# Kernel optimization log

Measured on AMD Instinct MI355X. Metric: run time of the kernel, lower is better.

Reference implementation:

```python
import jax, jax.numpy as jnp
import numpy as np
from jax import lax

K = 3
PAD = 1

def setup_inputs() -> dict:
    key = jax.random.key(0)
    ks = jax.random.split(key, 5)
    B, C, H, W, O = 4, 128, 128, 128, 256
    x = jax.random.normal(ks[0], (B, C, H, W), dtype=jnp.float32)
    w_off = jax.random.normal(ks[1], (3 * K * K, C, K, K), dtype=jnp.float32) * 0.05
    b_off = jnp.zeros((3 * K * K,), dtype=jnp.float32)
    w_dw = jax.random.normal(ks[2], (C, 1, K, K), dtype=jnp.float32) * 0.2
    b_dw = jnp.zeros((C,), dtype=jnp.float32)
    w_pw = jax.random.normal(ks[3], (O, C), dtype=jnp.float32) * (1.0 / np.sqrt(C))
    b_pw = jnp.zeros((O,), dtype=jnp.float32)
    return {"x": x, "w_off": w_off, "b_off": b_off, "w_dw": w_dw,
            "b_dw": b_dw, "w_pw": w_pw, "b_pw": b_pw}

def _dcn_forward(x, w_off, b_off, w_dw, b_dw, w_pw, b_pw):
    B, C, H, W = x.shape
    K2 = K * K
    # offset/mask conv (stride 1, pad 1) -> [B, 3*K*K, H, W]
    om = lax.conv_general_dilated(
        x, w_off, window_strides=(1, 1), padding=[(PAD, PAD), (PAD, PAD)],
        dimension_numbers=("NCHW", "OIHW", "NCHW")) + b_off[None, :, None, None]
    off = om[:, : 2 * K2]                      # [B, 2*K2, H, W]
    mask = jax.nn.sigmoid(om[:, 2 * K2:])      # [B, K2, H, W]
    dy = off[:, 0::2]                          # [B, K2, H, W] (y offsets)
    dx = off[:, 1::2]                          # [B, K2, H, W] (x offsets)
    # base sampling grid per kernel tap
    ky, kx = jnp.meshgrid(jnp.arange(K), jnp.arange(K), indexing="ij")
    ky = (ky.reshape(-1) - PAD).astype(x.dtype)   # [K2]
    kx = (kx.reshape(-1) - PAD).astype(x.dtype)
    py = jnp.arange(H, dtype=x.dtype)[None, None, :, None] + ky[None, :, None, None] + dy
    px = jnp.arange(W, dtype=x.dtype)[None, None, None, :] + kx[None, :, None, None] + dx
    y0 = jnp.floor(py); x0 = jnp.floor(px)
    wy = py - y0;       wx = px - x0

    def gather(yc, xc):
        # yc, xc: [B, K2, H, W] float corner coords; zero outside bounds
        valid = ((yc >= 0) & (yc < H) & (xc >= 0) & (xc < W)).astype(x.dtype)
        yi = jnp.clip(yc, 0, H - 1).astype(jnp.int32)
        xi = jnp.clip(xc, 0, W - 1).astype(jnp.int32)
        idx = yi * W + xi                       # [B, K2, H, W]
        def per_b(xb, ib):
            # xb: [C, H, W]; ib: [K2, H, W] -> [C, K2, H, W]
            return jnp.take(xb.reshape(C, -1), ib.reshape(-1), axis=1).reshape(C, K2, H, W)
        v = jax.vmap(per_b)(x, idx)             # [B, C, K2, H, W]
        return v * valid[:, None]

    val = (gather(y0, x0) * ((1 - wy) * (1 - wx))[:, None]
           + gather(y0, x0 + 1) * ((1 - wy) * wx)[:, None]
           + gather(y0 + 1, x0) * (wy * (1 - wx))[:, None]
           + gather(y0 + 1, x0 + 1) * (wy * wx)[:, None])  # [B, C, K2, H, W]
    val = val * mask[:, None]
    # depthwise deformable conv: per-channel K2 weights
    wk = w_dw.reshape(C, K2)
    out = jnp.einsum("bckhw,ck->bchw", val, wk) + b_dw[None, :, None, None]
    # pointwise 1x1 conv
    out = jnp.einsum("bchw,oc->bohw", out, w_pw) + b_pw[None, :, None, None]
    return out

def reference(x, w_off, b_off, w_dw, b_dw, w_pw, b_pw):
    return _dcn_forward(x, w_off, b_off, w_dw, b_dw, w_pw, b_pw)
```

## Files before the change

kernel.cpp:

```cpp
#include <hip/hip_runtime.h>
#include <hip/hip_bf16.h>
#include <math.h>

#define BB 4
#define CC 128
#define HH 128
#define WW 128
#define OO 256
#define HWP 16384

typedef __attribute__((ext_vector_type(8))) _Float16 half8;
typedef __attribute__((ext_vector_type(2))) _Float16 half2t;
typedef __attribute__((ext_vector_type(4))) float floatx4;

__device__ inline half2t u2h2(unsigned int u) {
  union { unsigned int i; half2t h; } z; z.i = u; return z.h;
}
__device__ inline unsigned short f2h_bits(float f) {
  union { _Float16 h; unsigned short s; } z; z.h = (_Float16)f; return z.s;
}

__device__ inline void blend2(unsigned int a00w, unsigned int a01w,
                              unsigned int a10w, unsigned int a11w,
                              half2t wt, half2t wb, float wk0, float wk1,
                              float& acc0, float& acc1) {
  unsigned int tl = __builtin_amdgcn_perm(a01w, a00w, 0x05040100u);
  unsigned int th = __builtin_amdgcn_perm(a01w, a00w, 0x07060302u);
  unsigned int bl = __builtin_amdgcn_perm(a11w, a10w, 0x05040100u);
  unsigned int bh = __builtin_amdgcn_perm(a11w, a10w, 0x07060302u);
  float v0 = __builtin_amdgcn_fdot2(u2h2(bl), wb, __builtin_amdgcn_fdot2(u2h2(tl), wt, 0.f, false), false);
  float v1 = __builtin_amdgcn_fdot2(u2h2(bh), wb, __builtin_amdgcn_fdot2(u2h2(th), wt, 0.f, false), false);
  acc0 = fmaf(v0, wk0, acc0);
  acc1 = fmaf(v1, wk1, acc1);
}

__device__ inline int om_idx(int px, int o) {
  return (((o >> 2) ^ (px & 7)) << 2) | (o & 3);
}

__global__ __launch_bounds__(256) void k_transpose(const float* __restrict__ x,
                                                   const float* __restrict__ w_off,
                                                   const float* __restrict__ w_pw,
                                                   unsigned int* __restrict__ xh32,
                                                   _Float16* __restrict__ Ah,
                                                   _Float16* __restrict__ Apw) {
  int tid = threadIdx.x;
  int bid = blockIdx.x;
  if (bid >= 1024) {
    int e = (bid - 1024) * 256 + tid;
    if (e < 144 * 32 * 8) {
      int kblk = e >> 8;
      int o = (e >> 3) & 31;
      int j = e & 7;
      int k = kblk * 8 + j;
      int t = k >> 7, c = k & 127;
      float w = (o < 27) ? w_off[(o * CC + c) * 9 + t] : 0.0f;
      Ah[e] = (_Float16)w;
    }
    int e2 = e - 144 * 32 * 8;
    if (e2 >= 0 && e2 < 16 * 256 * 8) {
      int cblk = e2 >> 11;
      int o = (e2 >> 3) & 255;
      int j = e2 & 7;
      Apw[e2] = (_Float16)w_pw[o * CC + cblk * 8 + j];
    }
    return;
  }
  __shared__ __align__(16) unsigned int tile32[64][64];
  int half = bid & 1;
  int h = (bid >> 1) & 127;
  int b = bid >> 8;
  int wq = tid & 15;
  int cb = tid >> 4;
#pragma unroll
  for (int i = 0; i < 4; i++) {
    int c0 = i * 32 + cb * 2;
    const float* p0 = x + ((size_t)(b * CC + c0) * HH + h) * WW + half * 64 + wq * 4;
    float4 v0 = *(const float4*)p0;
    float4 v1 = *(const float4*)(p0 + HWP);
    const float* f0 = &v0.x;
    const float* f1 = &v1.x;
    int cp = i * 16 + cb;
    int su = (cp >> 2) ^ wq;
#pragma unroll
    for (int j = 0; j < 4; j++) {
      unsigned int pk = (unsigned int)f2h_bits(f0[j]) | ((unsigned int)f2h_bits(f1[j]) << 16);
      tile32[wq * 4 + j][su * 4 + (cp & 3)] = pk;
    }
  }
  __syncthreads();
  int cg = tid & 15;
#pragma unroll
  for (int p = 0; p < 4; p++) {
    int w = p * 16 + (tid >> 4);
    int su = cg ^ ((w >> 2) & 15);
    uint4 v = *(const uint4*)&tile32[w][su * 4];
    *(uint4*)(xh32 + (size_t)((b * HH + h) * WW + half * 64 + w) * 64 + cg * 4) = v;
  }
}

__global__ __launch_bounds__(256, 4) void k_fused(
    const _Float16* __restrict__ xh, const _Float16* __restrict__ Ah,
    const _Float16* __restrict__ Apw, const float* __restrict__ b_off,
    const float* __restrict__ w_dw, const float* __restrict__ b_dw,
    const float* __restrict__ bpw, float* __restrict__ out) {
  __shared__ float om_s[32][32];
  __shared__ int s_packed[32][9];
  __shared__ unsigned int s_wp[32][9][2];
  __shared__ __align__(16) _Float16 val[32][128];

  int tid = threadIdx.x;
  int bid = blockIdx.x;
  int n0 = ((bid & 7) * 256 + (bid >> 3)) * 32;
  int b = n0 >> 14;
  int h0 = (n0 >> 7) & 127;
  int wbase = n0 & 127;

  int wv = tid >> 6, lane = tid & 63;
  int n16 = lane & 15, quad = lane >> 4;

  if (wv < 2) {
    int pxb = wv * 16;
    floatx4 acc0 = {}, acc1 = {};
    half8 zz = {};
#pragma unroll
    for (int t = 0; t < 9; t++) {
      int dy = t / 3 - 1, dx = t % 3 - 1;
      int hs = h0 + dy;
      bool hok = ((unsigned)hs < HH);
      int hsc = min(max(hs, 0), HH - 1);
      int wA = wbase + pxb + n16 + dx;
      bool okA = hok && ((unsigned)wA < WW);
      int wAc = min(max(wA, 0), WW - 1);
      size_t rowoff = (size_t)((b * HH + hsc) * WW + wAc) * CC + quad * 8;
#pragma unroll
      for (int cs = 0; cs < 4; cs++) {
        half8 bh = *(const half8*)(xh + rowoff + cs * 32);
        bh = okA ? bh : zz;
        int kblk = t * 16 + cs * 4 + quad;
        const _Float16* pa = Ah + (size_t)kblk * 256 + n16 * 8;
        half8 a0 = *(const half8*)pa;
        half8 a1 = *(const half8*)(pa + 128);
        __builtin_amdgcn_s_setprio(1);
        acc0 = __builtin_amdgcn_mfma_f32_16x16x32_f16(a0, bh, acc0, 0, 0, 0);
        acc1 = __builtin_amdgcn_mfma_f32_16x16x32_f16(a1, bh, acc1, 0, 0, 0);
        __builtin_amdgcn_s_setprio(0);
      }
    }
    int px = pxb + n16;
#pragma unroll
    for (int reg = 0; reg < 4; reg++) {
      int o0 = quad * 4 + reg;
      om_s[px][om_idx(px, o0)] = acc0[reg] + b_off[o0];
      int o1 = 16 + quad * 4 + reg;
      if (o1 < 27) om_s[px][om_idx(px, o1)] = acc1[reg] + b_off[o1];
    }
  }
  __syncthreads();

#pragma unroll
  for (int pass = 0; pass < 2; pass++) {
    int it = pass * 64 + lane;
    if (it < 72) {
      int pxl = it / 9;
      int k = it - pxl * 9;
      int px = wv * 8 + pxl;
      int w = wbase + px;
      float dyv = om_s[px][om_idx(px, 2 * k)];
      float dxv = om_s[px][om_idx(px, 2 * k + 1)];
      float mvv = om_s[px][om_idx(px, 18 + k)];
      mvv = 1.0f / (1.0f + __expf(-mvv));
      float py = (float)(h0 + k / 3 - 1) + dyv;
      float pxf = (float)(w + k % 3 - 1) + dxv;
      float y0f = floorf(py), x0f = floorf(pxf);
      float wy = py - y0f, wx = pxf - x0f;
      int y0 = (int)y0f, x0 = (int)x0f;
      int y1 = y0 + 1, x1 = x0 + 1;
      float v00 = (y0 >= 0 && y0 < HH && x0 >= 0 && x0 < WW) ? 1.f : 0.f;
      float v01 = (y0 >= 0 && y0 < HH && x1 >= 0 && x1 < WW) ? 1.f : 0.f;
      float v10 = (y1 >= 0 && y1 < HH && x0 >= 0 && x0 < WW) ? 1.f : 0.f;
      float v11 = (y1 >= 0 && y1 < HH && x1 >= 0 && x1 < WW) ? 1.f : 0.f;
      int y0c = min(max(y0, 0), HH - 1), y1c = min(max(y1, 0), HH - 1);
      int x0c = min(max(x0, 0), WW - 1), x1c = min(max(x1, 0), WW - 1);
      int base = ((b * HH + y0c) * WW + x0c) * CC;
      int dxf = (x1c > x0c) ? 1 : 0;
      int dyf = (y1c > y0c) ? 1 : 0;
      s_packed[px][k] = base | (dxf << 30) | (dyf << 31);
      float w00 = (1.f - wy) * (1.f - wx) * mvv * v00;
      float w01 = (1.f - wy) * wx * mvv * v01;
      float w10 = wy * (1.f - wx) * mvv * v10;
      float w11 = wy * wx * mvv * v11;
      s_wp[px][k][0] = (unsigned int)f2h_bits(w00) | ((unsigned int)f2h_bits(w01) << 16);
      s_wp[px][k][1] = (unsigned int)f2h_bits(w10) | ((unsigned int)f2h_bits(w11) << 16);
    }
  }

  {
    int c0 = lane * 2;
    const unsigned short* xs = (const unsigned short*)xh;
    float wk0[9], wk1[9];
    {
      const float* wp_ = w_dw + c0 * 9;
#pragma unroll
      for (int k = 0; k < 9; k++) { wk0[k] = wp_[k]; wk1[k] = wp_[9 + k]; }
    }
    float2 bdp = *(const float2*)(b_dw + c0);
    unsigned int voff = (unsigned int)(lane * 4);

#pragma unroll 1
    for (int p = 0; p < 8; p++) {
      int px = wv * 8 + p;
      unsigned int C00[9], C01[9], C10[9], C11[9];
#pragma unroll
      for (int k = 0; k < 9; k++) {
        int pk = __builtin_amdgcn_readfirstlane(s_packed[px][k]);
        unsigned long long b00 = (unsigned long long)xs + 2ull * (unsigned int)(pk & 0x3FFFFFFF);
        unsigned long long dxs = (pk & 0x40000000) ? (unsigned long long)(CC * 2) : 0ull;
        unsigned long long dys = (pk & 0x80000000u) ? (unsigned long long)(WW * CC * 2) : 0ull;
        unsigned long long b01 = b00 + dxs;
        unsigned long long b10 = b00 + dys;
        unsigned long long b11 = b10 + dxs;
        asm volatile("global_load_dword %0, %1, %2" : "=v"(C00[k]) : "v"(voff), "s"(b00));
        asm volatile("global_load_dword %0, %1, %2" : "=v"(C01[k]) : "v"(voff), "s"(b01));
        asm volatile("global_load_dword %0, %1, %2" : "=v"(C10[k]) : "v"(voff), "s"(b10));
        asm volatile("global_load_dword %0, %1, %2" : "=v"(C11[k]) : "v"(voff), "s"(b11));
      }
      asm volatile("s_waitcnt vmcnt(0)" ::: "memory");
      __builtin_amdgcn_sched_barrier(0);
      float a0 = 0.f, a1 = 0.f;
#pragma unroll
      for (int k = 0; k < 9; k++) {
        uint2 w2 = *(const uint2*)&s_wp[px][k][0];
        blend2(C00[k], C01[k], C10[k], C11[k], u2h2(w2.x), u2h2(w2.y),
               wk0[k], wk1[k], a0, a1);
      }
      unsigned int d = (unsigned int)f2h_bits(a0 + bdp.x) |
                       ((unsigned int)f2h_bits(a1 + bdp.y) << 16);
      int su = (lane >> 2) ^ (px & 7);
      *(unsigned int*)((char*)&val[px][0] + su * 16 + (lane & 3) * 4) = d;
    }
  }
  __syncthreads();

  {
    int obase = wv * 64;
    floatx4 acc[4][2] = {};
#pragma unroll
    for (int cs = 0; cs < 4; cs++) {
      half8 af[4], bf[2];
#pragma unroll
      for (int mf = 0; mf < 4; mf++) {
        const _Float16* pa = Apw + ((size_t)(cs * 4 + quad) * 256 + obase + mf * 16 + n16) * 8;
        af[mf] = *(const half8*)pa;
      }
#pragma unroll
      for (int nf = 0; nf < 2; nf++) {
        int row = nf * 16 + n16;
        int su = (cs * 4 + quad) ^ (row & 7);
        bf[nf] = *(const half8*)&val[row][su * 8];
      }
      __builtin_amdgcn_s_setprio(1);
#pragma unroll
      for (int mf = 0; mf < 4; mf++)
#pragma unroll
        for (int nf = 0; nf < 2; nf++)
          acc[mf][nf] = __builtin_amdgcn_mfma_f32_16x16x32_f16(af[mf], bf[nf], acc[mf][nf], 0, 0, 0);
      __builtin_amdgcn_s_setprio(0);
    }
#pragma unroll
    for (int mf = 0; mf < 4; mf++) {
#pragma unroll
      for (int reg = 0; reg < 4; reg++) {
        int o = obase + mf * 16 + quad * 4 + reg;
        float bo = bpw[o];
#pragma unroll
        for (int nf = 0; nf < 2; nf++) {
          int n = n0 + nf * 16 + n16;
          int hw = n & 16383;
          out[((size_t)(b * OO + o) << 14) + hw] = acc[mf][nf][reg] + bo;
        }
      }
    }
  }
}

extern "C" void kernel_launch(void* const* d_in, const int* in_sizes, int n_in,
                              void* d_out, int out_size, void* d_ws, size_t ws_size,
                              hipStream_t stream) {
  const float* x     = (const float*)d_in[0];
  const float* w_off = (const float*)d_in[1];
  const float* b_off = (const float*)d_in[2];
  const float* w_dw  = (const float*)d_in[3];
  const float* b_dw  = (const float*)d_in[4];
  const float* w_pw  = (const float*)d_in[5];
  const float* b_pw  = (const float*)d_in[6];
  float* out = (float*)d_out;
  float* ws  = (float*)d_ws;

  _Float16* xh  = (_Float16*)ws;
  _Float16* Ah  = (_Float16*)((char*)ws + 16777216);
  _Float16* Apw = Ah + 36864;

  k_transpose<<<1536, 256, 0, stream>>>(x, w_off, w_pw,
                                        (unsigned int*)xh, Ah, Apw);
  k_fused<<<2048, 256, 0, stream>>>(xh, Ah, Apw, b_off, w_dw, b_dw, b_pw, out);
}
```

Measured before the change: 159.9 us.

## Double-buffer deformable gather loads across pixels and shrink transpose blocks

The per-pixel bilinear gather loop now issues the 36 loads for the next pixel into an alternate register buffer before computing the current pixel. Partial vmcnt waits let memory latency overlap with the blend math. This doubles the gather register footprint, which could hurt occupancy under launch_bounds(256,4). Separately, the fp16 transpose kernel moves to 128-thread blocks covering 32 pixels each, with more blocks and a smaller LDS tile.

```diff
diff --git a/kernel.cpp b/kernel.cpp
--- a/kernel.cpp
+++ b/kernel.cpp
@@ -38,7 +38,7 @@
   return (((o >> 2) ^ (px & 7)) << 2) | (o & 3);
 }
 
-__global__ __launch_bounds__(256) void k_transpose(const float* __restrict__ x,
+__global__ __launch_bounds__(128) void k_transpose(const float* __restrict__ x,
                                                    const float* __restrict__ w_off,
                                                    const float* __restrict__ w_pw,
                                                    unsigned int* __restrict__ xh32,
@@ -46,8 +46,8 @@
                                                    _Float16* __restrict__ Apw) {
   int tid = threadIdx.x;
   int bid = blockIdx.x;
-  if (bid >= 1024) {
-    int e = (bid - 1024) * 256 + tid;
+  if (bid >= 2048) {
+    int e = (bid - 2048) * 128 + tid;
     if (e < 144 * 32 * 8) {
       int kblk = e >> 8;
       int o = (e >> 3) & 31;
@@ -66,21 +66,21 @@
     }
     return;
   }
-  __shared__ __align__(16) unsigned int tile32[64][64];
-  int half = bid & 1;
-  int h = (bid >> 1) & 127;
-  int b = bid >> 8;
-  int wq = tid & 15;
-  int cb = tid >> 4;
+  __shared__ __align__(16) unsigned int tile32[32][64];
+  int q = bid & 3;
+  int h = (bid >> 2) & 127;
+  int b = bid >> 9;
+  int wq = tid & 7;
+  int cb = tid >> 3;
 #pragma unroll
   for (int i = 0; i < 4; i++) {
-    int c0 = i * 32 + cb * 2;
-    const float* p0 = x + ((size_t)(b * CC + c0) * HH + h) * WW + half * 64 + wq * 4;
+    int cp = i * 16 + cb;
+    int c0 = cp * 2;
+    const float* p0 = x + ((size_t)(b * CC + c0) * HH + h) * WW + q * 32 + wq * 4;
     float4 v0 = *(const float4*)p0;
     float4 v1 = *(const float4*)(p0 + HWP);
     const float* f0 = &v0.x;
     const float* f1 = &v1.x;
-    int cp = i * 16 + cb;
     int su = (cp >> 2) ^ wq;
 #pragma unroll
     for (int j = 0; j < 4; j++) {
@@ -89,13 +89,14 @@
     }
   }
   __syncthreads();
-  int cg = tid & 15;
-#pragma unroll
-  for (int p = 0; p < 4; p++) {
-    int w = p * 16 + (tid >> 4);
-    int su = cg ^ ((w >> 2) & 15);
-    uint4 v = *(const uint4*)&tile32[w][su * 4];
-    *(uint4*)(xh32 + (size_t)((b * HH + h) * WW + half * 64 + w) * 64 + cg * 4) = v;
+  int px = tid >> 2;
+  int ur = tid & 3;
+#pragma unroll
+  for (int r = 0; r < 4; r++) {
+    int u = r * 4 + ur;
+    int su = u ^ ((px >> 2) & 7);
+    uint4 v = *(const uint4*)&tile32[px][su * 4];
+    *(uint4*)(xh32 + (size_t)((b * HH + h) * WW + q * 32 + px) * 64 + u * 4) = v;
   }
 }
 
@@ -207,37 +208,53 @@
     float2 bdp = *(const float2*)(b_dw + c0);
     unsigned int voff = (unsigned int)(lane * 4);
 
-#pragma unroll 1
-    for (int p = 0; p < 8; p++) {
-      int px = wv * 8 + p;
-      unsigned int C00[9], C01[9], C10[9], C11[9];
+#pragma unroll
+    for (int k = 0; k < 9; k++)
+      asm volatile("" :: "v"(wk0[k]), "v"(wk1[k]));
+    asm volatile("" :: "v"(bdp.x), "v"(bdp.y));
+    asm volatile("s_waitcnt vmcnt(0)" ::: "memory");
+
+    unsigned int Abuf[36], Bbuf[36];
+
+    auto issue_px = [&](int px, unsigned int* C) {
 #pragma unroll
       for (int k = 0; k < 9; k++) {
         int pk = __builtin_amdgcn_readfirstlane(s_packed[px][k]);
         unsigned long long b00 = (unsigned long long)xs + 2ull * (unsigned int)(pk & 0x3FFFFFFF);
         unsigned long long dxs = (pk & 0x40000000) ? (unsigned long long)(CC * 2) : 0ull;
         unsigned long long dys = (pk & 0x80000000u) ? (unsigned long long)(WW * CC * 2) : 0ull;
-        unsigned long long b01 = b00 + dxs;
-        unsigned long long b10 = b00 + dys;
-        unsigned long long b11 = b10 + dxs;
-        asm volatile("global_load_dword %0, %1, %2" : "=v"(C00[k]) : "v"(voff), "s"(b00));
-        asm volatile("global_load_dword %0, %1, %2" : "=v"(C01[k]) : "v"(voff), "s"(b01));
-        asm volatile("global_load_dword %0, %1, %2" : "=v"(C10[k]) : "v"(voff), "s"(b10));
-        asm volatile("global_load_dword %0, %1, %2" : "=v"(C11[k]) : "v"(voff), "s"(b11));
-      }
-      asm volatile("s_waitcnt vmcnt(0)" ::: "memory");
-      __builtin_amdgcn_sched_barrier(0);
+        asm volatile("global_load_dword %0, %1, %2" : "=v"(C[k * 4 + 0]) : "v"(voff), "s"(b00));
+        asm volatile("global_load_dword %0, %1, %2" : "=v"(C[k * 4 + 1]) : "v"(voff), "s"(b00 + dxs));
+        asm volatile("global_load_dword %0, %1, %2" : "=v"(C[k * 4 + 2]) : "v"(voff), "s"(b00 + dys));
+        asm volatile("global_load_dword %0, %1, %2" : "=v"(C[k * 4 + 3]) : "v"(voff), "s"(b00 + dys + dxs));
+      }
+    };
+    auto compute_px = [&](int px, const unsigned int* C) {
       float a0 = 0.f, a1 = 0.f;
 #pragma unroll
       for (int k = 0; k < 9; k++) {
         uint2 w2 = *(const uint2*)&s_wp[px][k][0];
-        blend2(C00[k], C01[k], C10[k], C11[k], u2h2(w2.x), u2h2(w2.y),
-               wk0[k], wk1[k], a0, a1);
+        blend2(C[k * 4 + 0], C[k * 4 + 1], C[k * 4 + 2], C[k * 4 + 3],
+               u2h2(w2.x), u2h2(w2.y), wk0[k], wk1[k], a0, a1);
       }
       unsigned int d = (unsigned int)f2h_bits(a0 + bdp.x) |
                        ((unsigned int)f2h_bits(a1 + bdp.y) << 16);
       int su = (lane >> 2) ^ (px & 7);
       *(unsigned int*)((char*)&val[px][0] + su * 16 + (lane & 3) * 4) = d;
+    };
+
+    issue_px(wv * 8 + 0, Abuf);
+#pragma unroll
+    for (int p = 0; p < 8; p++) {
+      int px = wv * 8 + p;
+      if (p < 7) {
+        issue_px(px + 1, (p & 1) ? Abuf : Bbuf);
+        asm volatile("s_waitcnt vmcnt(36)" ::: "memory");
+      } else {
+        asm volatile("s_waitcnt vmcnt(0)" ::: "memory");
+      }
+      __builtin_amdgcn_sched_barrier(0x100);
+      compute_px(px, (p & 1) ? Bbuf : Abuf);
     }
   }
   __syncthreads();
@@ -301,7 +318,7 @@
   _Float16* Ah  = (_Float16*)((char*)ws + 16777216);
   _Float16* Apw = Ah + 36864;
 
-  k_transpose<<<1536, 256, 0, stream>>>(x, w_off, w_pw,
+  k_transpose<<<2592, 128, 0, stream>>>(x, w_off, w_pw,
                                         (unsigned int*)xh, Ah, Apw);
   k_fused<<<2048, 256, 0, stream>>>(xh, Ah, Apw, b_off, w_dw, b_dw, b_pw, out);
 }
```

After: 162.2 us. No clear change (+1.4%).
